# Optimization experiments

Hardware: AMD Instinct MI355X
Metric: run time of the kernel (lower is better)

## Reference

```python
import jax, jax.numpy as jnp
import numpy as np

N, D, NH = 200000, 128, 8
B, S = 32, 512


def _build_levels():
    # Binary-tree DAG: parent(i) = (i-1)//2; level d = nodes [2^d-1, 2^(d+1)-1)
    levels = []
    d = 0
    while (2 ** d - 1) < N:
        lo, hi = 2 ** d - 1, min(2 ** (d + 1) - 1, N)
        levels.append(np.arange(lo, hi, dtype=np.int64))
        d += 1
    L = len(levels)
    M = max(len(l) for l in levels)
    child = np.full((L, M), N, dtype=np.int64)   # pad with dummy index N
    parent = np.full((L, M), N, dtype=np.int64)
    for i, l in enumerate(levels):
        child[i, : len(l)] = l
        parent[i, : len(l)] = np.where(l > 0, (l - 1) // 2, N)  # root -> dummy
    return child, parent


def setup_inputs() -> dict:
    key = jax.random.key(0)
    ks = jax.random.split(key, 4)
    child, parent = _build_levels()
    rng = np.random.default_rng(0)
    lengths = rng.integers(S // 2, S + 1, size=B)
    bidx = np.full((B, S), N, dtype=np.int64)  # dummy index N -> zero padding feats
    for b in range(B):
        bidx[b, : lengths[b]] = rng.integers(0, N, size=lengths[b])
    s = 1.0 / np.sqrt(D)
    return {
        "feats": jax.random.normal(ks[0], (N, D), jnp.float32),
        "in_proj_weight": jax.random.normal(ks[1], (3 * D, D), jnp.float32) * s,
        "in_proj_bias": jnp.zeros((3 * D,), jnp.float32),
        "out_proj_weight": jax.random.normal(ks[2], (D, D), jnp.float32) * s,
        "out_proj_bias": jnp.zeros((D,), jnp.float32),
        "levels_child": jnp.asarray(child),
        "levels_parent": jnp.asarray(parent),
        "branch_idx": jnp.asarray(bidx),
        "lengths": jnp.asarray(lengths.astype(np.int64)),
    }


def reference(feats, in_proj_weight, in_proj_bias, out_proj_weight, out_proj_bias,
              levels_child, levels_parent, branch_idx, lengths):
    n, d = feats.shape
    # --- dgl.prop_nodes_topo with PathAdd: feats[v] += feats[parent(v)], level by level ---
    f = jnp.concatenate([feats, jnp.zeros((1, d), feats.dtype)], axis=0)  # row N = dummy/pad (zeros)
    for i in range(levels_child.shape[0]):  # static number of topological levels
        f = f.at[levels_child[i]].add(f[levels_parent[i]])
    # --- gather branch features (offset_leaf) + pad_sequence(padding_value=0) ---
    x = f[branch_idx]  # [B,S,D]; dummy index gathers zeros
    b, s_len, _ = x.shape
    pos = jnp.arange(s_len)
    valid = (pos[None, :] < lengths[:, None]).astype(x.dtype)        # [B,S]
    mask = valid[:, :, None] * valid[:, None, :]                      # [B,S,S] float additive mask (1 valid, 0 pad)
    # --- nn.MultiheadAttention(batch_first=True) with float additive attn_mask ---
    qkv = x @ in_proj_weight.T + in_proj_bias                         # [B,S,3D]
    q, k, v = jnp.split(qkv, 3, axis=-1)
    hd = d // NH
    def sh(t):
        return t.reshape(b, s_len, NH, hd).transpose(0, 2, 1, 3)      # [B,H,S,hd]
    q, k, v = sh(q), sh(k), sh(v)
    scores = jnp.einsum('bhqd,bhkd->bhqk', q, k) * (1.0 / np.sqrt(hd)) + mask[:, None, :, :]
    attn = jax.nn.softmax(scores, axis=-1)
    o = jnp.einsum('bhqk,bhkd->bhqd', attn, v)
    o = o.transpose(0, 2, 1, 3).reshape(b, s_len, d)
    o = o @ out_proj_weight.T + out_proj_bias
    return jnp.sum(o, axis=1)  # torch.sum(out, dim=1) -> [B, D]
```

## Files before the change

kernel.cpp:

```cpp
#include <hip/hip_runtime.h>

#define NN 200000
#define DD 128
#define NHH 8
#define HD 16
#define BB 32
#define SS 512
#define QKV_LD 384

typedef __attribute__((ext_vector_type(8))) short short8;
typedef __attribute__((ext_vector_type(4))) float f32x4;

static __device__ __forceinline__ unsigned short f2bf(float f) {
    unsigned u = __float_as_uint(f);
    unsigned r = (u + 0x7FFFu + ((u >> 16) & 1u)) >> 16;
    return (unsigned short)r;
}
static __device__ __forceinline__ unsigned pk2(float a, float b) {
    return (unsigned)f2bf(a) | ((unsigned)f2bf(b) << 16);
}
static __device__ __forceinline__ unsigned cvtpk(float a, float b) {
    unsigned r;
    asm("v_cvt_pk_bf16_f32 %0, %1, %2" : "=v"(r) : "v"(a), "v"(b));
    return r;
}

__global__ __launch_bounds__(256) void k_gather(const float* __restrict__ feats,
                                                const int* __restrict__ bidx,
                                                unsigned short* __restrict__ xb) {
    int t = threadIdx.x;
    int r = t >> 5, c4 = t & 31;
    long row = (long)blockIdx.x * 8 + r;
    int idx = bidx[row];
    int v = (idx >= 0 && idx < NN) ? idx : NN;
    const float4* f4 = (const float4*)feats;
    int a[18];
    #pragma unroll
    for (int k = 0; k < 18; ++k) {
        a[k] = v;
        v = (v == 0 || v >= NN) ? NN : (v - 1) >> 1;
    }
    float4 val[18];
    float fl[18];
    #pragma unroll
    for (int k = 0; k < 18; ++k) {
        int aa = a[k] < NN ? a[k] : 0;
        fl[k] = a[k] < NN ? 1.f : 0.f;
        val[k] = f4[(long)aa * 32 + c4];
    }
    float4 acc = make_float4(0.f, 0.f, 0.f, 0.f);
    #pragma unroll
    for (int k = 0; k < 18; ++k) {
        acc.x += fl[k] * val[k].x; acc.y += fl[k] * val[k].y;
        acc.z += fl[k] * val[k].z; acc.w += fl[k] * val[k].w;
    }
    ushort4 o;
    o.x = f2bf(acc.x); o.y = f2bf(acc.y); o.z = f2bf(acc.z); o.w = f2bf(acc.w);
    ((ushort4*)xb)[row * 32 + c4] = o;
}

__global__ __launch_bounds__(256) void k_wconv(const float* __restrict__ W,
                                               unsigned short* __restrict__ Wb) {
    int i = (blockIdx.x * 256 + threadIdx.x) * 4;
    float4 v = *(const float4*)(W + i);
    ushort4 o;
    o.x = f2bf(v.x); o.y = f2bf(v.y); o.z = f2bf(v.z); o.w = f2bf(v.w);
    *(ushort4*)(Wb + i) = o;
}

__global__ __launch_bounds__(256) void k_qkv(const unsigned short* __restrict__ xb,
                                             const unsigned short* __restrict__ Wb,
                                             const float* __restrict__ bin,
                                             float* __restrict__ qkv) {
    __shared__ uint4 As4[128 * 16];
    __shared__ uint4 Bs4[128 * 16];
    int t = threadIdx.x;
    int rb = blockIdx.x / 3, cb = blockIdx.x % 3;
    long row0 = (long)rb * 128;
    int col0 = cb * 128;
    const uint4* ag = (const uint4*)xb + row0 * 16;
    const uint4* bg = (const uint4*)Wb + (long)col0 * 16;
    #pragma unroll
    for (int n = 0; n < 8; ++n) {
        int idx = n * 256 + t;
        int r = idx >> 4, c = idx & 15;
        int p = r * 16 + (c ^ (r & 15));
        As4[p] = ag[idx];
        Bs4[p] = bg[idx];
    }
    __syncthreads();

    int lane = t & 63, w = t >> 6;
    int wr = (w >> 1) * 64, wc = (w & 1) * 64;
    int frow = lane & 15, fk = lane >> 4;
    f32x4 acc[4][4] = {};
    const short8* A8 = (const short8*)As4;
    const short8* B8 = (const short8*)Bs4;
    #pragma unroll
    for (int ks = 0; ks < 4; ++ks) {
        int chunk = ks * 4 + fk;
        short8 af[4], bf[4];
        #pragma unroll
        for (int mi = 0; mi < 4; ++mi) {
            int r = wr + mi * 16 + frow;
            af[mi] = A8[r * 16 + (chunk ^ (r & 15))];
        }
        #pragma unroll
        for (int ni = 0; ni < 4; ++ni) {
            int r = wc + ni * 16 + frow;
            bf[ni] = B8[r * 16 + (chunk ^ (r & 15))];
        }
        #pragma unroll
        for (int mi = 0; mi < 4; ++mi)
            #pragma unroll
            for (int ni = 0; ni < 4; ++ni)
                acc[mi][ni] = __builtin_amdgcn_mfma_f32_16x16x32_bf16(
                    af[mi], bf[ni], acc[mi][ni], 0, 0, 0);
    }

    int rg = lane >> 4;
    #pragma unroll
    for (int ni = 0; ni < 4; ++ni) {
        int col = col0 + wc + ni * 16 + frow;
        float bb = bin[col];
        #pragma unroll
        for (int mi = 0; mi < 4; ++mi) {
            #pragma unroll
            for (int j = 0; j < 4; ++j) {
                long r = row0 + wr + mi * 16 + rg * 4 + j;
                qkv[r * QKV_LD + col] = acc[mi][ni][j] + bb;
            }
        }
    }
}

__global__ __launch_bounds__(256) void k_repack(const float* __restrict__ qkv,
                                                uint4* __restrict__ Qf,
                                                uint4* __restrict__ Kf,
                                                uint4* __restrict__ Vf,
                                                float* __restrict__ Vsum) {
    int bh = blockIdx.x, b = bh >> 3, h = bh & 7;
    int t = threadIdx.x;
    const float* base = qkv + (long)b * SS * QKV_LD;

    int l32 = t & 31, sub = t >> 5;
    int r16 = l32 & 15, g2 = l32 >> 4;
    #pragma unroll
    for (int pass = 0; pass < 4; ++pass) {
        int qt = pass * 8 + sub;
        const float* qp = base + (long)(qt * 16 + r16) * QKV_LD + h * HD + 8 * g2;
        float4 f0 = *(const float4*)qp;
        float4 f1 = *(const float4*)(qp + 4);
        uint4 uq;
        uq.x = pk2(f0.x * 0.25f, f0.y * 0.25f);
        uq.y = pk2(f0.z * 0.25f, f0.w * 0.25f);
        uq.z = pk2(f1.x * 0.25f, f1.y * 0.25f);
        uq.w = pk2(f1.z * 0.25f, f1.w * 0.25f);
        Qf[((long)bh * 32 + qt) * 32 + l32] = uq;
        const float* kp = qp + DD;
        float4 k0 = *(const float4*)kp;
        float4 k1 = *(const float4*)(kp + 4);
        uint4 uk;
        uk.x = pk2(k0.x, k0.y); uk.y = pk2(k0.z, k0.w);
        uk.z = pk2(k1.x, k1.y); uk.w = pk2(k1.z, k1.w);
        Kf[((long)bh * 32 + qt) * 32 + l32] = uk;
    }

    int lane = t & 63, vsub = t >> 6;
    int d = lane & 15, gg = lane >> 4;
    float vpart = 0.f;
    #pragma unroll
    for (int pass = 0; pass < 4; ++pass) {
        int kts = pass * 4 + vsub;
        int k0 = kts * 32 + gg * 8;
        float vv[8];
        #pragma unroll
        for (int i = 0; i < 8; ++i)
            vv[i] = base[(long)(k0 + i) * QKV_LD + 2 * DD + h * HD + d];
        #pragma unroll
        for (int i = 0; i < 8; ++i) vpart += vv[i];
        uint4 uv;
        uv.x = pk2(vv[0], vv[1]); uv.y = pk2(vv[2], vv[3]);
        uv.z = pk2(vv[4], vv[5]); uv.w = pk2(vv[6], vv[7]);
        Vf[((long)bh * 16 + kts) * 64 + lane] = uv;
    }
    __shared__ float vred[256];
    vred[t] = vpart;
    __syncthreads();
    if (t < HD) {
        float s = 0.f;
        #pragma unroll
        for (int j = 0; j < 16; ++j) s += vred[t + j * 16];
        Vsum[bh * HD + t] = s;
    }
}

__global__ __launch_bounds__(256) void k_attn(const uint4* __restrict__ Qf,
                                              const uint4* __restrict__ Kf,
                                              const uint4* __restrict__ Vf,
                                              const int* __restrict__ lengths,
                                              float* __restrict__ tpart) {
    int blk = blockIdx.x;
    int bh = blk >> 1, half = blk & 1;
    int b = bh >> 3;
    int t = threadIdx.x, lane = t & 63, w = t >> 6;
    int len = lengths[b];
    int q15 = lane & 15, g = lane >> 4;
    int nsup = (len + 31) >> 5;
    int ntk = nsup * 2;

    __shared__ unsigned pbuf[4][256];
    __shared__ float red[4][HD];
    unsigned* pw = &pbuf[w][0];

    float osum[4] = {0.f, 0.f, 0.f, 0.f};
    const uint4 z4 = make_uint4(0u, 0u, 0u, 0u);

    #pragma unroll
    for (int i = 0; i < 4; ++i) {
        int qt = half * 16 + w * 4 + i;
        if (qt * 16 >= len) continue;

        uint4 qfu = (lane < 32) ? Qf[((long)bh * 32 + qt) * 32 + lane] : z4;
        short8 qf = __builtin_bit_cast(short8, qfu);

        f32x4 sacc[32];
        #pragma unroll
        for (int kt = 0; kt < 32; ++kt) {
            if (kt < ntk) {
                uint4 kfu = (lane < 32) ? Kf[((long)bh * 32 + kt) * 32 + lane] : z4;
                f32x4 cz = {0.f, 0.f, 0.f, 0.f};
                sacc[kt] = __builtin_amdgcn_mfma_f32_16x16x32_bf16(
                    __builtin_bit_cast(short8, kfu), qf, cz, 0, 0, 0);
            }
        }
        #pragma unroll
        for (int kt = 0; kt < 32; ++kt) {
            if (kt < ntk && kt * 16 + 15 >= len) {
                #pragma unroll
                for (int j = 0; j < 4; ++j) {
                    int tok = kt * 16 + g * 4 + j;
                    sacc[kt][j] = (tok < len) ? sacc[kt][j] : -1e30f;
                }
            }
        }
        float m = -1.0f;
        #pragma unroll
        for (int kt = 0; kt < 32; ++kt)
            if (kt < ntk)
                m = fmaxf(m, fmaxf(fmaxf(sacc[kt][0], sacc[kt][1]),
                                   fmaxf(sacc[kt][2], sacc[kt][3])));
        m = fmaxf(m, __shfl_xor(m, 16, 64));
        m = fmaxf(m, __shfl_xor(m, 32, 64));

        float l = 0.f;
        f32x4 oacc = {0.f, 0.f, 0.f, 0.f};
        #pragma unroll
        for (int kts = 0; kts < 16; ++kts) {
            if (kts < nsup) {
                f32x4 s0 = sacc[2 * kts], s1 = sacc[2 * kts + 1];
                float p00 = __expf(s0[0] - m), p01 = __expf(s0[1] - m);
                float p02 = __expf(s0[2] - m), p03 = __expf(s0[3] - m);
                float p10 = __expf(s1[0] - m), p11 = __expf(s1[1] - m);
                float p12 = __expf(s1[2] - m), p13 = __expf(s1[3] - m);
                l += ((p00 + p01) + (p02 + p03)) + ((p10 + p11) + (p12 + p13));
                unsigned u0 = cvtpk(p00, p01), u1 = cvtpk(p02, p03);
                unsigned u2 = cvtpk(p10, p11), u3 = cvtpk(p12, p13);
                *(uint2*)&pw[q15 * 16 + 2 * g]     = make_uint2(u0, u1);
                *(uint2*)&pw[q15 * 16 + 8 + 2 * g] = make_uint2(u2, u3);
                uint4 bfr = *(uint4*)&pw[q15 * 16 + 4 * g];
                uint4 vfu = Vf[((long)bh * 16 + kts) * 64 + lane];
                oacc = __builtin_amdgcn_mfma_f32_16x16x32_bf16(
                    __builtin_bit_cast(short8, vfu),
                    __builtin_bit_cast(short8, bfr), oacc, 0, 0, 0);
            }
        }
        l += __shfl_xor(l, 16, 64);
        l += __shfl_xor(l, 32, 64);
        float tl = l + (float)(SS - len) * __expf(-1.0f - m);
        int q = qt * 16 + q15;
        float inv = (q < len) ? 1.0f / tl : 0.0f;
        #pragma unroll
        for (int j = 0; j < 4; ++j) osum[j] += oacc[j] * inv;
    }

    #pragma unroll
    for (int j = 0; j < 4; ++j) {
        float v = osum[j];
        v += __shfl_xor(v, 1, 64);
        v += __shfl_xor(v, 2, 64);
        v += __shfl_xor(v, 4, 64);
        v += __shfl_xor(v, 8, 64);
        osum[j] = v;
    }
    if (q15 == 0) {
        #pragma unroll
        for (int j = 0; j < 4; ++j) red[w][g * 4 + j] = osum[j];
    }
    __syncthreads();
    if (t < HD)
        tpart[blk * HD + t] = red[0][t] + red[1][t] + red[2][t] + red[3][t];
}

__global__ __launch_bounds__(DD) void k_out(const float* __restrict__ tpart,
                                            const float* __restrict__ Vsum,
                                            const int* __restrict__ lengths,
                                            const float* __restrict__ Wout,
                                            const float* __restrict__ bout,
                                            float* __restrict__ out) {
    int b = blockIdx.x;
    int d = threadIdx.x;
    int len = lengths[b];
    __shared__ float tr[DD];
    int bh = b * 8 + (d >> 4), dd = d & 15;
    float inv_q = (float)(SS - len) * (1.0f / (float)SS);
    tr[d] = tpart[(bh * 2 + 0) * HD + dd] + tpart[(bh * 2 + 1) * HD + dd]
          + inv_q * Vsum[bh * HD + dd];
    __syncthreads();
    float s = (float)SS * bout[d];
    #pragma unroll 8
    for (int c = 0; c < DD; ++c) s += tr[c] * Wout[d * DD + c];
    out[b * DD + d] = s;
}

extern "C" void kernel_launch(void* const* d_in, const int* in_sizes, int n_in,
                              void* d_out, int out_size, void* d_ws, size_t ws_size,
                              hipStream_t stream) {
    const float* feats = (const float*)d_in[0];
    const float* Win   = (const float*)d_in[1];
    const float* bin   = (const float*)d_in[2];
    const float* Wout  = (const float*)d_in[3];
    const float* bout  = (const float*)d_in[4];
    const int* bidx    = (const int*)d_in[7];
    const int* lengths = (const int*)d_in[8];
    float* out = (float*)d_out;

    char* ws = (char*)d_ws;
    unsigned short* xb = (unsigned short*)ws;
    uint4* Vf          = (uint4*)ws;
    unsigned short* Wb = (unsigned short*)(ws + 4194304);
    float* qkv         = (float*)(ws + 8388608);
    uint4* Qf          = (uint4*)(ws + 33554432);
    uint4* Kf          = (uint4*)(ws + 37748736);
    float* Vsum        = (float*)(ws + 41943040);
    float* tpart       = (float*)(ws + 41959424);

    k_gather<<<BB * SS / 8, 256, 0, stream>>>(feats, bidx, xb);
    k_wconv<<<48, 256, 0, stream>>>(Win, Wb);
    k_qkv<<<128 * 3, 256, 0, stream>>>(xb, Wb, bin, qkv);
    k_repack<<<BB * NHH, 256, 0, stream>>>(qkv, Qf, Kf, Vf, Vsum);
    k_attn<<<BB * NHH * 2, 256, 0, stream>>>(Qf, Kf, Vf, lengths, tpart);
    k_out<<<BB, DD, 0, stream>>>(tpart, Vsum, lengths, Wout, bout, out);
}
```

Measured before the change: 268.9 us.

## Recompute scores in two passes, permute K to drop LDS staging, fuse weight convert

The attention kernel no longer holds all 32 score tiles in registers. It computes the row max in a first pass over K, then recomputes the scores in a second pass fused with exp and the PV MFMA. This lowers register pressure and raises occupancy, at the cost of doing the QK^T MFMAs twice. The K repack now permutes token order so that the softmax probabilities from the MFMA output can feed the PV MFMA directly without an LDS round-trip. The grid also splits each head into four query-tile groups instead of two, and the separate weight-to-bf16 conversion kernel is folded into the QKV GEMM tile load.

Measured after the change: 217.6 us. 19.1% less time.

```diff
diff --git a/kernel.cpp b/kernel.cpp
--- a/kernel.cpp
+++ b/kernel.cpp
@@ -59,17 +59,8 @@
     ((ushort4*)xb)[row * 32 + c4] = o;
 }
 
-__global__ __launch_bounds__(256) void k_wconv(const float* __restrict__ W,
-                                               unsigned short* __restrict__ Wb) {
-    int i = (blockIdx.x * 256 + threadIdx.x) * 4;
-    float4 v = *(const float4*)(W + i);
-    ushort4 o;
-    o.x = f2bf(v.x); o.y = f2bf(v.y); o.z = f2bf(v.z); o.w = f2bf(v.w);
-    *(ushort4*)(Wb + i) = o;
-}
-
 __global__ __launch_bounds__(256) void k_qkv(const unsigned short* __restrict__ xb,
-                                             const unsigned short* __restrict__ Wb,
+                                             const float* __restrict__ Win,
                                              const float* __restrict__ bin,
                                              float* __restrict__ qkv) {
     __shared__ uint4 As4[128 * 16];
@@ -79,14 +70,18 @@
     long row0 = (long)rb * 128;
     int col0 = cb * 128;
     const uint4* ag = (const uint4*)xb + row0 * 16;
-    const uint4* bg = (const uint4*)Wb + (long)col0 * 16;
     #pragma unroll
     for (int n = 0; n < 8; ++n) {
         int idx = n * 256 + t;
         int r = idx >> 4, c = idx & 15;
-        int p = r * 16 + (c ^ (r & 15));
-        As4[p] = ag[idx];
-        Bs4[p] = bg[idx];
+        As4[r * 16 + (c ^ (r & 15))] = ag[idx];
+        const float* wp = Win + (long)(col0 + r) * DD + c * 8;
+        float4 f0 = *(const float4*)wp;
+        float4 f1 = *(const float4*)(wp + 4);
+        uint4 u;
+        u.x = pk2(f0.x, f0.y); u.y = pk2(f0.z, f0.w);
+        u.z = pk2(f1.x, f1.y); u.w = pk2(f1.z, f1.w);
+        Bs4[r * 16 + (c ^ (r & 15))] = u;
     }
     __syncthreads();
 
@@ -157,7 +152,8 @@
         uq.z = pk2(f1.x * 0.25f, f1.y * 0.25f);
         uq.w = pk2(f1.z * 0.25f, f1.w * 0.25f);
         Qf[((long)bh * 32 + qt) * 32 + l32] = uq;
-        const float* kp = qp + DD;
+        int ktok = ((qt >> 1) << 5) + ((r16 >> 2) << 3) + ((qt & 1) << 2) + (r16 & 3);
+        const float* kp = base + (long)ktok * QKV_LD + DD + h * HD + 8 * g2;
         float4 k0 = *(const float4*)kp;
         float4 k1 = *(const float4*)(kp + 4);
         uint4 uk;
@@ -201,7 +197,7 @@
                                               const int* __restrict__ lengths,
                                               float* __restrict__ tpart) {
     int blk = blockIdx.x;
-    int bh = blk >> 1, half = blk & 1;
+    int bh = blk >> 2, qq = blk & 3;
     int b = bh >> 3;
     int t = threadIdx.x, lane = t & 63, w = t >> 6;
     int len = lengths[b];
@@ -209,77 +205,72 @@
     int nsup = (len + 31) >> 5;
     int ntk = nsup * 2;
 
-    __shared__ unsigned pbuf[4][256];
+    const uint4* Qb = Qf + (long)bh * 32 * 32;
+    const uint4* Kb = Kf + (long)bh * 32 * 32;
+    const uint4* Vb = Vf + (long)bh * 16 * 64;
     __shared__ float red[4][HD];
-    unsigned* pw = &pbuf[w][0];
+    const uint4 z4 = make_uint4(0u, 0u, 0u, 0u);
+    const f32x4 cz = {0.f, 0.f, 0.f, 0.f};
 
     float osum[4] = {0.f, 0.f, 0.f, 0.f};
-    const uint4 z4 = make_uint4(0u, 0u, 0u, 0u);
-
-    #pragma unroll
-    for (int i = 0; i < 4; ++i) {
-        int qt = half * 16 + w * 4 + i;
+
+    #pragma unroll
+    for (int i = 0; i < 2; ++i) {
+        int qt = qq + 4 * w + 16 * i;
         if (qt * 16 >= len) continue;
 
-        uint4 qfu = (lane < 32) ? Qf[((long)bh * 32 + qt) * 32 + lane] : z4;
+        uint4 qfu = (lane < 32) ? Qb[qt * 32 + lane] : z4;
         short8 qf = __builtin_bit_cast(short8, qfu);
 
-        f32x4 sacc[32];
-        #pragma unroll
-        for (int kt = 0; kt < 32; ++kt) {
-            if (kt < ntk) {
-                uint4 kfu = (lane < 32) ? Kf[((long)bh * 32 + kt) * 32 + lane] : z4;
-                f32x4 cz = {0.f, 0.f, 0.f, 0.f};
-                sacc[kt] = __builtin_amdgcn_mfma_f32_16x16x32_bf16(
+        float m = -1.0f;
+        for (int kt = 0; kt < ntk; kt += 4) {
+            #pragma unroll
+            for (int u = 0; u < 4; ++u) {
+                int k2 = (kt + u < ntk) ? kt + u : ntk - 1;
+                uint4 kfu = (lane < 32) ? Kb[k2 * 32 + lane] : z4;
+                f32x4 s = __builtin_amdgcn_mfma_f32_16x16x32_bf16(
                     __builtin_bit_cast(short8, kfu), qf, cz, 0, 0, 0);
+                m = fmaxf(m, fmaxf(fmaxf(s[0], s[1]), fmaxf(s[2], s[3])));
             }
         }
-        #pragma unroll
-        for (int kt = 0; kt < 32; ++kt) {
-            if (kt < ntk && kt * 16 + 15 >= len) {
+        m = fmaxf(m, __shfl_xor(m, 16, 64));
+        m = fmaxf(m, __shfl_xor(m, 32, 64));
+
+        float l = 0.f;
+        f32x4 oacc = {0.f, 0.f, 0.f, 0.f};
+        bool strad = (len & 31) != 0;
+        for (int kts = 0; kts < nsup; ++kts) {
+            uint4 k0u = (lane < 32) ? Kb[(2 * kts) * 32 + lane] : z4;
+            uint4 k1u = (lane < 32) ? Kb[(2 * kts + 1) * 32 + lane] : z4;
+            f32x4 s0 = __builtin_amdgcn_mfma_f32_16x16x32_bf16(
+                __builtin_bit_cast(short8, k0u), qf, cz, 0, 0, 0);
+            f32x4 s1 = __builtin_amdgcn_mfma_f32_16x16x32_bf16(
+                __builtin_bit_cast(short8, k1u), qf, cz, 0, 0, 0);
+            if (kts == nsup - 1 && strad) {
+                int tb = kts * 32 + 8 * g;
                 #pragma unroll
                 for (int j = 0; j < 4; ++j) {
-                    int tok = kt * 16 + g * 4 + j;
-                    sacc[kt][j] = (tok < len) ? sacc[kt][j] : -1e30f;
+                    s0[j] = (tb + j < len) ? s0[j] : -1e30f;
+                    s1[j] = (tb + 4 + j < len) ? s1[j] : -1e30f;
                 }
             }
-        }
-        float m = -1.0f;
-        #pragma unroll
-        for (int kt = 0; kt < 32; ++kt)
-            if (kt < ntk)
-                m = fmaxf(m, fmaxf(fmaxf(sacc[kt][0], sacc[kt][1]),
-                                   fmaxf(sacc[kt][2], sacc[kt][3])));
-        m = fmaxf(m, __shfl_xor(m, 16, 64));
-        m = fmaxf(m, __shfl_xor(m, 32, 64));
-
-        float l = 0.f;
-        f32x4 oacc = {0.f, 0.f, 0.f, 0.f};
-        #pragma unroll
-        for (int kts = 0; kts < 16; ++kts) {
-            if (kts < nsup) {
-                f32x4 s0 = sacc[2 * kts], s1 = sacc[2 * kts + 1];
-                float p00 = __expf(s0[0] - m), p01 = __expf(s0[1] - m);
-                float p02 = __expf(s0[2] - m), p03 = __expf(s0[3] - m);
-                float p10 = __expf(s1[0] - m), p11 = __expf(s1[1] - m);
-                float p12 = __expf(s1[2] - m), p13 = __expf(s1[3] - m);
-                l += ((p00 + p01) + (p02 + p03)) + ((p10 + p11) + (p12 + p13));
-                unsigned u0 = cvtpk(p00, p01), u1 = cvtpk(p02, p03);
-                unsigned u2 = cvtpk(p10, p11), u3 = cvtpk(p12, p13);
-                *(uint2*)&pw[q15 * 16 + 2 * g]     = make_uint2(u0, u1);
-                *(uint2*)&pw[q15 * 16 + 8 + 2 * g] = make_uint2(u2, u3);
-                uint4 bfr = *(uint4*)&pw[q15 * 16 + 4 * g];
-                uint4 vfu = Vf[((long)bh * 16 + kts) * 64 + lane];
-                oacc = __builtin_amdgcn_mfma_f32_16x16x32_bf16(
-                    __builtin_bit_cast(short8, vfu),
-                    __builtin_bit_cast(short8, bfr), oacc, 0, 0, 0);
-            }
+            float p0 = __expf(s0[0] - m), p1 = __expf(s0[1] - m);
+            float p2 = __expf(s0[2] - m), p3 = __expf(s0[3] - m);
+            float p4 = __expf(s1[0] - m), p5 = __expf(s1[1] - m);
+            float p6 = __expf(s1[2] - m), p7 = __expf(s1[3] - m);
+            l += ((p0 + p1) + (p2 + p3)) + ((p4 + p5) + (p6 + p7));
+            uint4 pf;
+            pf.x = cvtpk(p0, p1); pf.y = cvtpk(p2, p3);
+            pf.z = cvtpk(p4, p5); pf.w = cvtpk(p6, p7);
+            uint4 vfu = Vb[kts * 64 + lane];
+            oacc = __builtin_amdgcn_mfma_f32_16x16x32_bf16(
+                __builtin_bit_cast(short8, vfu),
+                __builtin_bit_cast(short8, pf), oacc, 0, 0, 0);
         }
         l += __shfl_xor(l, 16, 64);
         l += __shfl_xor(l, 32, 64);
         float tl = l + (float)(SS - len) * __expf(-1.0f - m);
-        int q = qt * 16 + q15;
-        float inv = (q < len) ? 1.0f / tl : 0.0f;
+        float inv = (qt * 16 + q15 < len) ? 1.0f / tl : 0.0f;
         #pragma unroll
         for (int j = 0; j < 4; ++j) osum[j] += oacc[j] * inv;
     }
@@ -314,8 +305,9 @@
     __shared__ float tr[DD];
     int bh = b * 8 + (d >> 4), dd = d & 15;
     float inv_q = (float)(SS - len) * (1.0f / (float)SS);
-    tr[d] = tpart[(bh * 2 + 0) * HD + dd] + tpart[(bh * 2 + 1) * HD + dd]
-          + inv_q * Vsum[bh * HD + dd];
+    float s4 = tpart[(bh * 4 + 0) * HD + dd] + tpart[(bh * 4 + 1) * HD + dd]
+             + tpart[(bh * 4 + 2) * HD + dd] + tpart[(bh * 4 + 3) * HD + dd];
+    tr[d] = s4 + inv_q * Vsum[bh * HD + dd];
     __syncthreads();
     float s = (float)SS * bout[d];
     #pragma unroll 8
@@ -338,17 +330,15 @@
     char* ws = (char*)d_ws;
     unsigned short* xb = (unsigned short*)ws;
     uint4* Vf          = (uint4*)ws;
-    unsigned short* Wb = (unsigned short*)(ws + 4194304);
+    float* Vsum        = (float*)(ws + 4194304);
+    float* tpart       = (float*)(ws + 4259840);
     float* qkv         = (float*)(ws + 8388608);
     uint4* Qf          = (uint4*)(ws + 33554432);
     uint4* Kf          = (uint4*)(ws + 37748736);
-    float* Vsum        = (float*)(ws + 41943040);
-    float* tpart       = (float*)(ws + 41959424);
 
     k_gather<<<BB * SS / 8, 256, 0, stream>>>(feats, bidx, xb);
-    k_wconv<<<48, 256, 0, stream>>>(Win, Wb);
-    k_qkv<<<128 * 3, 256, 0, stream>>>(xb, Wb, bin, qkv);
+    k_qkv<<<128 * 3, 256, 0, stream>>>(xb, Win, bin, qkv);
     k_repack<<<BB * NHH, 256, 0, stream>>>(qkv, Qf, Kf, Vf, Vsum);
-    k_attn<<<BB * NHH * 2, 256, 0, stream>>>(Qf, Kf, Vf, lengths, tpart);
+    k_attn<<<BB * NHH * 4, 256, 0, stream>>>(Qf, Kf, Vf, lengths, tpart);
     k_out<<<BB, DD, 0, stream>>>(tpart, Vsum, lengths, Wout, bout, out);
 }
```
